# Optimization experiments

Hardware: AMD Instinct MI355X
Metric: run time of the kernel (lower is better)

The kernel has to match this reference:

```python
import jax, jax.numpy as jnp
import numpy as np

EPS = 1e-10


def setup_inputs() -> dict:
    key = jax.random.key(0)
    kS, kQ, kW, kL = jax.random.split(key, 4)
    B, C, K, Q, D = 64, 20, 5, 15, 2048
    support = jax.random.normal(kS, (B * C * K, D), dtype=jnp.float32)
    query = jax.random.normal(kQ, (B * C * Q, D), dtype=jnp.float32)
    # encoder = single Linear(in_dim=D, hidden=D)
    W = jax.random.normal(kW, (D, D), dtype=jnp.float32) / np.sqrt(D)
    b = jnp.zeros((D,), dtype=jnp.float32)
    # one-hot support labels: each class appears K times per episode
    labels = jax.random.randint(kL, (B, C * K), 0, C)
    support_label_one_hot = jax.nn.one_hot(labels, C, dtype=jnp.float32)
    return {
        "support": support,
        "query": query,
        "support_label_one_hot": support_label_one_hot,
        "W": W,
        "b": b,
        "C": C,
        "K": K,
        "Q": Q,
    }


def reference(support, query, support_label_one_hot, W, b, C, K, Q):
    H = W.shape[1]
    # encoder (linear) on flat batches
    s = (support @ W + b).reshape(-1, C * K, H)   # [B, C*K, H]
    q = (query @ W + b).reshape(-1, C * Q, H)     # [B, C*Q, H]
    # DistanceNetwork: cosine-like similarity, only support magnitude normalized
    inv_norm = jax.lax.rsqrt(jnp.clip(jnp.sum(s * s, axis=-1), EPS, None))  # [B, C*K]
    sim = jnp.einsum("bqh,bsh->bqs", q, s) * inv_norm[:, None, :]           # [B, C*Q, C*K]
    # AttentionClassify: softmax over support set, then weighted sum of one-hot labels
    att = jax.nn.softmax(sim, axis=-1)                                       # [B, C*Q, C*K]
    preds = jnp.einsum("bqs,bsc->bqc", att, support_label_one_hot)          # [B, C*Q, C]
    probs = preds.reshape(-1, C)                                             # [B*C*Q, C]
    pred = jnp.argmax(probs, axis=1)
    return probs, pred
```

## Files before the change

### kernel.cpp

```cpp
#include <hip/hip_runtime.h>
#include <hip/hip_bf16.h>
#include <math.h>

#define BATCH 64
#define NCLS  20
#define NS    100
#define NQ    300
#define DIM   2048
#define MS    (BATCH * NS)
#define MQ    (BATCH * NQ)
#define KSPL  4
#define PROW  320
#define PCOL  112

typedef __attribute__((ext_vector_type(8))) short frag_ab;
typedef __attribute__((ext_vector_type(4))) float frag_cd;

union FAB { frag_ab f; unsigned u[4]; };

__device__ __forceinline__ unsigned rne_hi(float x) {
  unsigned u = __float_as_uint(x);
  return (u + 0x7FFFu + ((u >> 16) & 1u)) & 0xFFFF0000u;
}

__device__ __forceinline__ void split2rn(float x, float y, unsigned& p1,
                                         unsigned& p2) {
  union { __hip_bfloat162 h; unsigned u; } c1, c2;
  c1.h = __float22bfloat162_rn(make_float2(x, y));
  p1 = c1.u;
  float rx = x - __uint_as_float(c1.u << 16);
  float ry = y - __uint_as_float(c1.u & 0xFFFF0000u);
  c2.h = __float22bfloat162_rn(make_float2(rx, ry));
  p2 = c2.u;
}

#define GLL16(g, l)                                                            \
  __builtin_amdgcn_global_load_lds(                                            \
      (const __attribute__((address_space(1))) void*)(g),                      \
      (__attribute__((address_space(3))) void*)(l), 16, 0, 0)

__global__ __launch_bounds__(256) void esplit2(const float* __restrict__ X,
                                               unsigned short* __restrict__ X1,
                                               unsigned short* __restrict__ X2,
                                               int n4) {
  int i = blockIdx.x * 256 + threadIdx.x;
  if (i >= n4) return;
  float4 v = ((const float4*)X)[i];
  float x[4] = {v.x, v.y, v.z, v.w};
  ushort4 o1, o2;
  unsigned short* d1 = (unsigned short*)&o1;
  unsigned short* d2 = (unsigned short*)&o2;
#pragma unroll
  for (int q = 0; q < 4; ++q) {
    unsigned u1 = rne_hi(x[q]);
    float r1 = x[q] - __uint_as_float(u1);
    unsigned u2 = rne_hi(r1);
    d1[q] = (unsigned short)(u1 >> 16);
    d2[q] = (unsigned short)(u2 >> 16);
  }
  ((ushort4*)X1)[i] = o1;
  ((ushort4*)X2)[i] = o2;
}

template <int NH, int MINW>
__global__ __launch_bounds__(256, MINW) void gemm_bb3(
    const unsigned short* __restrict__ A1, const unsigned short* __restrict__ A2,
    const unsigned short* __restrict__ B1, const unsigned short* __restrict__ B2,
    float* __restrict__ Y, unsigned short* __restrict__ S1o,
    unsigned short* __restrict__ S2o) {
  __shared__ __align__(16) unsigned short A1s[4][128][8];
  __shared__ __align__(16) unsigned short A2s[4][128][8];
  __shared__ __align__(16) unsigned short B1s[4][128 * NH][8];
  __shared__ __align__(16) unsigned short B2s[4][128 * NH][8];

  const int tid = threadIdx.x;
  const int w = tid >> 6, lane = tid & 63;
  const int ml = lane & 15, kq = lane >> 4;
  const int wm = (w >> 1) * 64, wn = (w & 1) * 64;
  const int col0 = blockIdx.x * (128 * NH), row0 = blockIdx.y * 128;

  frag_cd acc[NH][4][4];
#pragma unroll
  for (int h = 0; h < NH; ++h)
#pragma unroll
    for (int i = 0; i < 4; ++i)
#pragma unroll
      for (int j = 0; j < 4; ++j)
#pragma unroll
        for (int r = 0; r < 4; ++r) acc[h][i][j][r] = 0.f;

  for (int k0 = 0; k0 < DIM; k0 += 32) {
#pragma unroll
    for (int mh = 0; mh < 2; ++mh) {
      const size_t off = (size_t)(row0 + mh * 64 + lane) * DIM + k0 + w * 8;
      GLL16(A1 + off, &A1s[w][mh * 64][0]);
      GLL16(A2 + off, &A2s[w][mh * 64][0]);
    }
#pragma unroll
    for (int t = 0; t < 2 * NH; ++t) {
      const size_t off = (size_t)(col0 + t * 64 + lane) * DIM + k0 + w * 8;
      GLL16(B1 + off, &B1s[w][t * 64][0]);
      GLL16(B2 + off, &B2s[w][t * 64][0]);
    }
    __syncthreads();

    FAB a1[4], a2[4];
#pragma unroll
    for (int i = 0; i < 4; ++i) {
      int m = wm + i * 16 + ml;
      *(uint4*)&a1[i].u[0] = *(const uint4*)&A1s[kq][m][0];
      *(uint4*)&a2[i].u[0] = *(const uint4*)&A2s[kq][m][0];
    }
#pragma unroll
    for (int nh = 0; nh < NH; ++nh) {
#pragma unroll
      for (int j = 0; j < 4; ++j) {
        int n = nh * 128 + wn + j * 16 + ml;
        FAB b1, b2;
        *(uint4*)&b1.u[0] = *(const uint4*)&B1s[kq][n][0];
        *(uint4*)&b2.u[0] = *(const uint4*)&B2s[kq][n][0];
#pragma unroll
        for (int i = 0; i < 4; ++i) {
          acc[nh][i][j] = __builtin_amdgcn_mfma_f32_16x16x32_bf16(
              a1[i].f, b1.f, acc[nh][i][j], 0, 0, 0);
          acc[nh][i][j] = __builtin_amdgcn_mfma_f32_16x16x32_bf16(
              a1[i].f, b2.f, acc[nh][i][j], 0, 0, 0);
          acc[nh][i][j] = __builtin_amdgcn_mfma_f32_16x16x32_bf16(
              a2[i].f, b1.f, acc[nh][i][j], 0, 0, 0);
        }
      }
    }
    __syncthreads();
  }

#pragma unroll
  for (int nh = 0; nh < NH; ++nh)
#pragma unroll
    for (int j = 0; j < 4; ++j) {
      int col = col0 + nh * 128 + wn + j * 16 + ml;
#pragma unroll
      for (int i = 0; i < 4; ++i) {
        int rowb = row0 + wm + i * 16 + kq * 4;
#pragma unroll
        for (int r = 0; r < 4; ++r) {
          float val = acc[nh][i][j][r];
          size_t idx = (size_t)(rowb + r) * DIM + col;
          if (Y) Y[idx] = val;
          unsigned u1 = rne_hi(val);
          float rr = val - __uint_as_float(u1);
          unsigned u2 = rne_hi(rr);
          S1o[idx] = (unsigned short)(u1 >> 16);
          S2o[idx] = (unsigned short)(u2 >> 16);
        }
      }
    }
}

#define MFMA3(ACC, A1, A2, BV1, BV2)                                           \
  ACC = __builtin_amdgcn_mfma_f32_16x16x32_bf16(A1.f, BV1.f, ACC, 0, 0, 0);    \
  ACC = __builtin_amdgcn_mfma_f32_16x16x32_bf16(A1.f, BV2.f, ACC, 0, 0, 0);    \
  ACC = __builtin_amdgcn_mfma_f32_16x16x32_bf16(A2.f, BV1.f, ACC, 0, 0, 0)

#define SIMJ(J)                                                                \
  {                                                                            \
    FAB bf1, bf2;                                                              \
    *(uint4*)&bf1.u[0] = *(const uint4*)(z1b + o##J + k0);                     \
    *(uint4*)&bf2.u[0] = *(const uint4*)(z2b + o##J + k0);                     \
    MFMA3(acc##J, a1, a2, bf1, bf2);                                           \
  }

#define STJ(J)                                                                 \
  {                                                                            \
    const int n = J * 16 + ml;                                                 \
    part[pbase + 0 * PCOL + n] = acc##J[0];                                    \
    part[pbase + 1 * PCOL + n] = acc##J[1];                                    \
    part[pbase + 2 * PCOL + n] = acc##J[2];                                    \
    part[pbase + 3 * PCOL + n] = acc##J[3];                                    \
  }

__global__ __launch_bounds__(256) void sim2_part(
    const float* __restrict__ Xq, const unsigned short* __restrict__ Z1,
    const unsigned short* __restrict__ Z2, const float* __restrict__ wb,
    float* __restrict__ part, float* __restrict__ upart) {
  const int wg = blockIdx.x + 5 * blockIdx.y + 320 * blockIdx.z;
  const int swz = (wg & 7) * 160 + (wg >> 3);
  const int b = swz / 20;
  const int r20 = swz % 20;
  const int ks = r20 / 5;
  const int mt = r20 % 5;

  const int w = threadIdx.x >> 6, lane = threadIdx.x & 63;
  const int ml = lane & 15, kq = lane >> 4;

  int r = mt * 64 + w * 16 + ml;
  const int rc = r < NQ ? r : NQ - 1;
  const float* aptr = Xq + ((size_t)b * NQ + rc) * DIM + kq * 8;

  const unsigned short* z1b = Z1 + (size_t)b * NS * DIM + kq * 8;
  const unsigned short* z2b = Z2 + (size_t)b * NS * DIM + kq * 8;
  const int o0 = (0 * 16 + ml) * DIM;
  const int o1 = (1 * 16 + ml) * DIM;
  const int o2 = (2 * 16 + ml) * DIM;
  const int o3 = (3 * 16 + ml) * DIM;
  const int o4 = (4 * 16 + ml) * DIM;
  const int o5 = (5 * 16 + ml) * DIM;
  const int n6 = 6 * 16 + ml;
  const int o6 = (n6 < NS ? n6 : NS - 1) * DIM;

  frag_cd acc0 = {0.f, 0.f, 0.f, 0.f}, acc1 = {0.f, 0.f, 0.f, 0.f};
  frag_cd acc2 = {0.f, 0.f, 0.f, 0.f}, acc3 = {0.f, 0.f, 0.f, 0.f};
  frag_cd acc4 = {0.f, 0.f, 0.f, 0.f}, acc5 = {0.f, 0.f, 0.f, 0.f};
  frag_cd acc6 = {0.f, 0.f, 0.f, 0.f};
  float up = 0.f;

  const int kbeg = ks * (DIM / KSPL), kend = kbeg + DIM / KSPL;
#pragma unroll 2
  for (int k0 = kbeg; k0 < kend; k0 += 32) {
    float4 f0 = *(const float4*)(aptr + k0);
    float4 f1 = *(const float4*)(aptr + k0 + 4);
    float4 wa = *(const float4*)(wb + k0 + kq * 8);
    float4 wc = *(const float4*)(wb + k0 + kq * 8 + 4);
    up += f0.x * wa.x + f0.y * wa.y + f0.z * wa.z + f0.w * wa.w +
          f1.x * wc.x + f1.y * wc.y + f1.z * wc.z + f1.w * wc.w;
    FAB a1, a2;
    split2rn(f0.x, f0.y, a1.u[0], a2.u[0]);
    split2rn(f0.z, f0.w, a1.u[1], a2.u[1]);
    split2rn(f1.x, f1.y, a1.u[2], a2.u[2]);
    split2rn(f1.z, f1.w, a1.u[3], a2.u[3]);
    SIMJ(0); SIMJ(1); SIMJ(2); SIMJ(3); SIMJ(4); SIMJ(5); SIMJ(6);
  }

  up += __shfl_xor(up, 16, 64);
  up += __shfl_xor(up, 32, 64);
  if (lane < 16)
    upart[((size_t)ks * BATCH + b) * PROW + mt * 64 + w * 16 + ml] = up;

  const size_t pbase =
      (((size_t)ks * BATCH + b) * PROW + (mt * 64 + w * 16 + kq * 4)) * PCOL;
  STJ(0); STJ(1); STJ(2); STJ(3); STJ(4); STJ(5); STJ(6);
}

__global__ __launch_bounds__(256) void gemv_wb(const float* __restrict__ W,
                                               const float* __restrict__ b,
                                               float* __restrict__ wb,
                                               float* __restrict__ bb) {
  const int k = blockIdx.x;
  const int d0 = threadIdx.x * 8;
  float4 w0 = *(const float4*)(W + (size_t)k * DIM + d0);
  float4 w1 = *(const float4*)(W + (size_t)k * DIM + d0 + 4);
  float4 b0 = *(const float4*)(b + d0);
  float4 b1 = *(const float4*)(b + d0 + 4);
  float s = w0.x * b0.x + w0.y * b0.y + w0.z * b0.z + w0.w * b0.w +
            w1.x * b1.x + w1.y * b1.y + w1.z * b1.z + w1.w * b1.w;
#pragma unroll
  for (int off = 32; off; off >>= 1) s += __shfl_down(s, off, 64);
  __shared__ float red[4];
  if ((threadIdx.x & 63) == 0) red[threadIdx.x >> 6] = s;
  __syncthreads();
  if (threadIdx.x == 0) wb[k] = red[0] + red[1] + red[2] + red[3];
  if (k == 0) {
    float s2 = b0.x * b0.x + b0.y * b0.y + b0.z * b0.z + b0.w * b0.w +
               b1.x * b1.x + b1.y * b1.y + b1.z * b1.z + b1.w * b1.w;
#pragma unroll
    for (int off = 32; off; off >>= 1) s2 += __shfl_down(s2, off, 64);
    __syncthreads();
    if ((threadIdx.x & 63) == 0) red[threadIdx.x >> 6] = s2;
    __syncthreads();
    if (threadIdx.x == 0) bb[0] = red[0] + red[1] + red[2] + red[3];
  }
}

__global__ __launch_bounds__(256) void norm_v(const float* __restrict__ Z,
                                              const float* __restrict__ Xs,
                                              const float* __restrict__ wb,
                                              const float* __restrict__ bb,
                                              float* __restrict__ inv_norm,
                                              float* __restrict__ vv) {
  const int row = blockIdx.x;
  const int d0 = threadIdx.x * 8;
  const float* zp = Z + (size_t)row * DIM + d0;
  const float* xp = Xs + (size_t)row * DIM + d0;
  float4 z0 = *(const float4*)zp, z1 = *(const float4*)(zp + 4);
  float4 x0 = *(const float4*)xp, x1 = *(const float4*)(xp + 4);
  float4 w0 = *(const float4*)(wb + d0), w1 = *(const float4*)(wb + d0 + 4);
  float s1 = z0.x * x0.x + z0.y * x0.y + z0.z * x0.z + z0.w * x0.w +
             z1.x * x1.x + z1.y * x1.y + z1.z * x1.z + z1.w * x1.w;
  float s2 = x0.x * w0.x + x0.y * w0.y + x0.z * w0.z + x0.w * w0.w +
             x1.x * w1.x + x1.y * w1.y + x1.z * w1.z + x1.w * w1.w;
#pragma unroll
  for (int off = 32; off; off >>= 1) {
    s1 += __shfl_down(s1, off, 64);
    s2 += __shfl_down(s2, off, 64);
  }
  __shared__ float r1[4], r2[4];
  if ((threadIdx.x & 63) == 0) {
    r1[threadIdx.x >> 6] = s1;
    r2[threadIdx.x >> 6] = s2;
  }
  __syncthreads();
  if (threadIdx.x == 0) {
    float t1 = r1[0] + r1[1] + r1[2] + r1[3];
    float t2 = r2[0] + r2[1] + r2[2] + r2[3];
    float nn = t1 + 2.f * t2 + bb[0];
    inv_norm[row] = rsqrtf(fmaxf(nn, 1e-10f));
    vv[row] = t2;
  }
}

__global__ __launch_bounds__(256) void softmax_part(
    const float* __restrict__ part, const float* __restrict__ upart,
    const float* __restrict__ vv, const float* __restrict__ bb,
    const float* __restrict__ inv_norm, const float* __restrict__ onehot,
    float* __restrict__ out) {
  const int wave = threadIdx.x >> 6;
  const int lane = threadIdx.x & 63;
  const int r = blockIdx.x * 4 + wave;
  const int b = r / NQ;
  const int m = r - b * NQ;
  const size_t kstr = (size_t)BATCH * PROW * PCOL;
  const size_t ustr = (size_t)BATCH * PROW;
  const float* p0 = part + ((size_t)b * PROW + m) * PCOL;
  const float* up0 = upart + (size_t)b * PROW + m;
  const float bbv = bb[0];
  const float ur = up0[0] + up0[ustr] + up0[2 * ustr] + up0[3 * ustr];

  float raw1 = p0[lane] + p0[kstr + lane] + p0[2 * kstr + lane] +
               p0[3 * kstr + lane];
  float v1 = (raw1 + ur + vv[b * NS + lane] + bbv) * inv_norm[b * NS + lane];
  float v2 = -INFINITY;
  if (lane < NS - 64) {
    const int n = lane + 64;
    float raw2 = p0[n] + p0[kstr + n] + p0[2 * kstr + n] + p0[3 * kstr + n];
    v2 = (raw2 + ur + vv[b * NS + n] + bbv) * inv_norm[b * NS + n];
  }
  float mx = fmaxf(v1, v2);
#pragma unroll
  for (int off = 32; off; off >>= 1) mx = fmaxf(mx, __shfl_xor(mx, off, 64));
  float e1 = expf(v1 - mx);
  float e2 = (lane < NS - 64) ? expf(v2 - mx) : 0.f;
  float ssum = e1 + e2;
#pragma unroll
  for (int off = 32; off; off >>= 1) ssum += __shfl_xor(ssum, off, 64);
  float inv = 1.0f / ssum;
  __shared__ float att[4][NS];
  __shared__ float pr[4][NCLS];
  att[wave][lane] = e1 * inv;
  if (lane < NS - 64) att[wave][lane + 64] = e2 * inv;
  __syncthreads();
  if (lane < NCLS) {
    const float* oh = onehot + ((size_t)b * NS) * NCLS + lane;
    float p = 0.f;
#pragma unroll 4
    for (int j = 0; j < NS; ++j) p += att[wave][j] * oh[(size_t)j * NCLS];
    out[(size_t)r * NCLS + lane] = p;
    pr[wave][lane] = p;
  }
  __syncthreads();
  if (lane == 0) {
    int best = 0;
    float bv = pr[wave][0];
    for (int c = 1; c < NCLS; ++c) {
      float v = pr[wave][c];
      if (v > bv) { bv = v; best = c; }
    }
    out[(size_t)MQ * NCLS + r] = (float)best;
  }
}

__global__ __launch_bounds__(256) void softmax_fb(
    const float* __restrict__ sim, const float* __restrict__ onehot,
    float* __restrict__ out) {
  const int wave = threadIdx.x >> 6;
  const int lane = threadIdx.x & 63;
  const int r = blockIdx.x * 4 + wave;
  const int b = r / NQ;
  const float* srow = sim + (size_t)r * NS;
  float v1 = srow[lane];
  float v2 = (lane < NS - 64) ? srow[lane + 64] : -INFINITY;
  float m = fmaxf(v1, v2);
#pragma unroll
  for (int off = 32; off; off >>= 1) m = fmaxf(m, __shfl_xor(m, off, 64));
  float e1 = expf(v1 - m);
  float e2 = (lane < NS - 64) ? expf(v2 - m) : 0.f;
  float ssum = e1 + e2;
#pragma unroll
  for (int off = 32; off; off >>= 1) ssum += __shfl_xor(ssum, off, 64);
  float inv = 1.0f / ssum;
  __shared__ float att[4][NS];
  __shared__ float pr[4][NCLS];
  att[wave][lane] = e1 * inv;
  if (lane < NS - 64) att[wave][lane + 64] = e2 * inv;
  __syncthreads();
  if (lane < NCLS) {
    const float* oh = onehot + ((size_t)b * NS) * NCLS + lane;
    float p = 0.f;
#pragma unroll 4
    for (int j = 0; j < NS; ++j) p += att[wave][j] * oh[(size_t)j * NCLS];
    out[(size_t)r * NCLS + lane] = p;
    pr[wave][lane] = p;
  }
  __syncthreads();
  if (lane == 0) {
    int best = 0;
    float bv = pr[wave][0];
    for (int c = 1; c < NCLS; ++c) {
      float v = pr[wave][c];
      if (v > bv) { bv = v; best = c; }
    }
    out[(size_t)MQ * NCLS + r] = (float)best;
  }
}

__global__ __launch_bounds__(256) void gemm_xw(const float* __restrict__ X,
                                               const float* __restrict__ W,
                                               const float* __restrict__ bias,
                                               float* __restrict__ Y) {
  __shared__ float As[16][64];
  __shared__ float Bs[16][64];
  const int t = threadIdx.x;
  const int row0 = blockIdx.x * 64;
  const int col0 = blockIdx.y * 64;
  const int am = t >> 2, ak = (t & 3) * 4;
  const int bk = t >> 4, bn = (t & 15) * 4;
  const int tm = (t >> 4) * 4, tn = (t & 15) * 4;
  float acc[4][4] = {};
  for (int k0 = 0; k0 < DIM; k0 += 16) {
    float4 av = *(const float4*)(X + (size_t)(row0 + am) * DIM + k0 + ak);
    As[ak + 0][am] = av.x;
    As[ak + 1][am] = av.y;
    As[ak + 2][am] = av.z;
    As[ak + 3][am] = av.w;
    *(float4*)&Bs[bk][bn] =
        *(const float4*)(W + (size_t)(k0 + bk) * DIM + col0 + bn);
    __syncthreads();
#pragma unroll
    for (int k = 0; k < 16; ++k) {
      float4 a4 = *(const float4*)&As[k][tm];
      float4 b4 = *(const float4*)&Bs[k][tn];
      float av_[4] = {a4.x, a4.y, a4.z, a4.w};
      float bv_[4] = {b4.x, b4.y, b4.z, b4.w};
#pragma unroll
      for (int i = 0; i < 4; ++i)
#pragma unroll
        for (int j = 0; j < 4; ++j) acc[i][j] += av_[i] * bv_[j];
    }
    __syncthreads();
  }
  float4 bbv = *(const float4*)(bias + col0 + tn);
  float bv_[4] = {bbv.x, bbv.y, bbv.z, bbv.w};
#pragma unroll
  for (int i = 0; i < 4; ++i) {
    float4 o;
    o.x = acc[i][0] + bv_[0];
    o.y = acc[i][1] + bv_[1];
    o.z = acc[i][2] + bv_[2];
    o.w = acc[i][3] + bv_[3];
    *(float4*)(Y + (size_t)(row0 + tm + i) * DIM + col0 + tn) = o;
  }
}

__global__ __launch_bounds__(256) void norm_kernel(const float* __restrict__ s,
                                                   float* __restrict__ inv_norm) {
  const int row = blockIdx.x;
  const float* p = s + (size_t)row * DIM;
  const int d0 = threadIdx.x * 8;
  float4 a = *(const float4*)(p + d0);
  float4 b = *(const float4*)(p + d0 + 4);
  float sum = a.x * a.x + a.y * a.y + a.z * a.z + a.w * a.w +
              b.x * b.x + b.y * b.y + b.z * b.z + b.w * b.w;
#pragma unroll
  for (int off = 32; off; off >>= 1) sum += __shfl_down(sum, off, 64);
  __shared__ float red[4];
  if ((threadIdx.x & 63) == 0) red[threadIdx.x >> 6] = sum;
  __syncthreads();
  if (threadIdx.x == 0) {
    float tot = red[0] + red[1] + red[2] + red[3];
    inv_norm[row] = rsqrtf(fmaxf(tot, 1e-10f));
  }
}

__global__ __launch_bounds__(256) void sim_kernel(const float* __restrict__ q,
                                                  const float* __restrict__ s,
                                                  const float* __restrict__ inv_norm,
                                                  float* __restrict__ sim) {
  __shared__ float As[16][64];
  __shared__ float Bs[16][64];
  const int t = threadIdx.x;
  const int b = blockIdx.z;
  const int row0 = blockIdx.y * 64;
  const int col0 = blockIdx.x * 64;
  const float* qb = q + (size_t)b * NQ * DIM;
  const float* sb = s + (size_t)b * NS * DIM;
  const int am = t >> 2, ak = (t & 3) * 4;
  const int tm = (t >> 4) * 4, tn = (t & 15) * 4;
  float acc[4][4] = {};
  for (int k0 = 0; k0 < DIM; k0 += 16) {
    float4 av = make_float4(0.f, 0.f, 0.f, 0.f);
    if (row0 + am < NQ)
      av = *(const float4*)(qb + (size_t)(row0 + am) * DIM + k0 + ak);
    As[ak + 0][am] = av.x;
    As[ak + 1][am] = av.y;
    As[ak + 2][am] = av.z;
    As[ak + 3][am] = av.w;
    float4 bv = make_float4(0.f, 0.f, 0.f, 0.f);
    if (col0 + am < NS)
      bv = *(const float4*)(sb + (size_t)(col0 + am) * DIM + k0 + ak);
    Bs[ak + 0][am] = bv.x;
    Bs[ak + 1][am] = bv.y;
    Bs[ak + 2][am] = bv.z;
    Bs[ak + 3][am] = bv.w;
    __syncthreads();
#pragma unroll
    for (int k = 0; k < 16; ++k) {
      float4 a4 = *(const float4*)&As[k][tm];
      float4 b4 = *(const float4*)&Bs[k][tn];
      float av_[4] = {a4.x, a4.y, a4.z, a4.w};
      float bv_[4] = {b4.x, b4.y, b4.z, b4.w};
#pragma unroll
      for (int i = 0; i < 4; ++i)
#pragma unroll
        for (int j = 0; j < 4; ++j) acc[i][j] += av_[i] * bv_[j];
    }
    __syncthreads();
  }
#pragma unroll
  for (int i = 0; i < 4; ++i) {
    int m = row0 + tm + i;
    if (m >= NQ) continue;
#pragma unroll
    for (int j = 0; j < 4; ++j) {
      int n = col0 + tn + j;
      if (n >= NS) continue;
      sim[((size_t)b * NQ + m) * NS + n] = acc[i][j] * inv_norm[b * NS + n];
    }
  }
}

extern "C" void kernel_launch(void* const* d_in, const int* in_sizes, int n_in,
                              void* d_out, int out_size, void* d_ws,
                              size_t ws_size, hipStream_t stream) {
  const float* support = (const float*)d_in[0];
  const float* query   = (const float*)d_in[1];
  const float* onehot  = (const float*)d_in[2];
  const float* W       = (const float*)d_in[3];
  const float* bias    = (const float*)d_in[4];

  char* wsb = (char*)d_ws;

  const size_t NEED = 191228160;

  if (ws_size >= NEED) {
    float* Z              = (float*)wsb;
    unsigned short* S1    = (unsigned short*)(wsb + (size_t)52428800);
    unsigned short* S2    = (unsigned short*)(wsb + (size_t)78643200);
    unsigned short* Wr1   = (unsigned short*)(wsb + (size_t)104857600);
    unsigned short* Wr2   = (unsigned short*)(wsb + (size_t)113246208);
    unsigned short* G1    = (unsigned short*)(wsb + (size_t)121634816);
    unsigned short* G2    = (unsigned short*)(wsb + (size_t)130023424);
    unsigned short* Z1    = (unsigned short*)(wsb + (size_t)138412032);
    unsigned short* Z2    = (unsigned short*)(wsb + (size_t)164626432);
    float* part           = (float*)(wsb + (size_t)52428800);
    float* inv_norm       = (float*)(wsb + (size_t)190840832);
    float* vv             = (float*)(wsb + (size_t)190866432);
    float* wb             = (float*)(wsb + (size_t)190892032);
    float* bb             = (float*)(wsb + (size_t)190900224);
    float* upart          = (float*)(wsb + (size_t)190900480);

    esplit2<<<DIM * DIM / 1024, 256, 0, stream>>>(W, Wr1, Wr2, DIM * DIM / 4);
    esplit2<<<MS * DIM / 1024, 256, 0, stream>>>(support, S1, S2,
                                                 MS * DIM / 4);
    gemm_bb3<1, 2><<<dim3(DIM / 128, DIM / 128), 256, 0, stream>>>(
        Wr1, Wr2, Wr1, Wr2, nullptr, G1, G2);
    gemm_bb3<2, 2><<<dim3(DIM / 256, MS / 128), 256, 0, stream>>>(
        S1, S2, G1, G2, Z, Z1, Z2);
    gemv_wb<<<DIM, 256, 0, stream>>>(W, bias, wb, bb);
    norm_v<<<MS, 256, 0, stream>>>(Z, support, wb, bb, inv_norm, vv);
    sim2_part<<<dim3(5, BATCH, KSPL), 256, 0, stream>>>(query, Z1, Z2, wb,
                                                        part, upart);
    softmax_part<<<MQ / 4, 256, 0, stream>>>(part, upart, vv, bb, inv_norm,
                                             onehot, (float*)d_out);
  } else {
    float* s = (float*)wsb;
    float* q = (float*)(wsb + (size_t)52428800);
    float* inv_norm = q + (size_t)MQ * DIM;
    float* sim      = inv_norm + MS;
    gemm_xw<<<dim3(MS / 64, DIM / 64), 256, 0, stream>>>(support, W, bias, s);
    gemm_xw<<<dim3(MQ / 64, DIM / 64), 256, 0, stream>>>(query, W, bias, q);
    norm_kernel<<<MS, 256, 0, stream>>>(s, inv_norm);
    sim_kernel<<<dim3(2, 5, BATCH), 256, 0, stream>>>(q, s, inv_norm, sim);
    softmax_fb<<<MQ / 4, 256, 0, stream>>>(sim, onehot, (float*)d_out);
  }
}
```

Baseline: 747.8 us.

## Fuse W split with bias GEMV, drop fp32 Z, swizzle GEMM tiles

Merges the W bf16 split with the W·b GEMV into one kernel, so W is read once instead of twice. The support GEMM no longer writes an fp32 Z; the norm kernel instead rebuilds Z from its bf16 hi/lo pair, which removes a large write and read at a small precision cost. The GEMMs gain a grouped workgroup-index swizzle for L2 locality, and the second GEMM drops from 256-wide to 128-wide tiles while the occupancy hint rises to 4. The workspace layout shrinks accordingly.

```diff
diff --git a/kernel.cpp b/kernel.cpp
--- a/kernel.cpp
+++ b/kernel.cpp
@@ -32,6 +32,10 @@
   float ry = y - __uint_as_float(c1.u & 0xFFFF0000u);
   c2.h = __float22bfloat162_rn(make_float2(rx, ry));
   p2 = c2.u;
+}
+
+__device__ __forceinline__ float bf16_f(unsigned short s) {
+  return __uint_as_float(((unsigned)s) << 16);
 }
 
 #define GLL16(g, l)                                                            \
@@ -62,6 +66,60 @@
   ((ushort4*)X2)[i] = o2;
 }
 
+__global__ __launch_bounds__(256) void esplit2w(const float* __restrict__ W,
+                                                const float* __restrict__ b,
+                                                unsigned short* __restrict__ W1,
+                                                unsigned short* __restrict__ W2,
+                                                float* __restrict__ wb,
+                                                float* __restrict__ bb) {
+  const int row = blockIdx.x;
+  const int d0 = threadIdx.x * 8;
+  const float* wr = W + (size_t)row * DIM + d0;
+  float4 x0 = *(const float4*)wr, x1 = *(const float4*)(wr + 4);
+  float4 b0 = *(const float4*)(b + d0), b1 = *(const float4*)(b + d0 + 4);
+  float xs[8] = {x0.x, x0.y, x0.z, x0.w, x1.x, x1.y, x1.z, x1.w};
+  ushort4 o1a, o2a, o1b, o2b;
+  unsigned short* p1a = (unsigned short*)&o1a;
+  unsigned short* p2a = (unsigned short*)&o2a;
+  unsigned short* p1b = (unsigned short*)&o1b;
+  unsigned short* p2b = (unsigned short*)&o2b;
+#pragma unroll
+  for (int q = 0; q < 4; ++q) {
+    unsigned u1 = rne_hi(xs[q]);
+    float r1 = xs[q] - __uint_as_float(u1);
+    unsigned u2 = rne_hi(r1);
+    p1a[q] = (unsigned short)(u1 >> 16);
+    p2a[q] = (unsigned short)(u2 >> 16);
+    unsigned v1 = rne_hi(xs[q + 4]);
+    float r2 = xs[q + 4] - __uint_as_float(v1);
+    unsigned v2 = rne_hi(r2);
+    p1b[q] = (unsigned short)(v1 >> 16);
+    p2b[q] = (unsigned short)(v2 >> 16);
+  }
+  *(ushort4*)&W1[(size_t)row * DIM + d0] = o1a;
+  *(ushort4*)&W1[(size_t)row * DIM + d0 + 4] = o1b;
+  *(ushort4*)&W2[(size_t)row * DIM + d0] = o2a;
+  *(ushort4*)&W2[(size_t)row * DIM + d0 + 4] = o2b;
+  float s = x0.x * b0.x + x0.y * b0.y + x0.z * b0.z + x0.w * b0.w +
+            x1.x * b1.x + x1.y * b1.y + x1.z * b1.z + x1.w * b1.w;
+#pragma unroll
+  for (int off = 32; off; off >>= 1) s += __shfl_down(s, off, 64);
+  __shared__ float red[4];
+  if ((threadIdx.x & 63) == 0) red[threadIdx.x >> 6] = s;
+  __syncthreads();
+  if (threadIdx.x == 0) wb[row] = red[0] + red[1] + red[2] + red[3];
+  if (row == 0) {
+    float s2 = b0.x * b0.x + b0.y * b0.y + b0.z * b0.z + b0.w * b0.w +
+               b1.x * b1.x + b1.y * b1.y + b1.z * b1.z + b1.w * b1.w;
+#pragma unroll
+    for (int off = 32; off; off >>= 1) s2 += __shfl_down(s2, off, 64);
+    __syncthreads();
+    if ((threadIdx.x & 63) == 0) red[threadIdx.x >> 6] = s2;
+    __syncthreads();
+    if (threadIdx.x == 0) bb[0] = red[0] + red[1] + red[2] + red[3];
+  }
+}
+
 template <int NH, int MINW>
 __global__ __launch_bounds__(256, MINW) void gemm_bb3(
     const unsigned short* __restrict__ A1, const unsigned short* __restrict__ A2,
@@ -77,7 +135,14 @@
   const int w = tid >> 6, lane = tid & 63;
   const int ml = lane & 15, kq = lane >> 4;
   const int wm = (w >> 1) * 64, wn = (w & 1) * 64;
-  const int col0 = blockIdx.x * (128 * NH), row0 = blockIdx.y * 128;
+
+  const int nwgx = gridDim.x;
+  const int nwg = nwgx * gridDim.y;
+  const int wg = blockIdx.x + nwgx * blockIdx.y;
+  const int qq = nwg >> 3;
+  const int swz = (wg & 7) * qq + (wg >> 3);
+  const int col0 = (swz % nwgx) * (128 * NH);
+  const int row0 = (swz / nwgx) * 128;
 
   frag_cd acc[NH][4][4];
 #pragma unroll
@@ -240,51 +305,24 @@
   STJ(0); STJ(1); STJ(2); STJ(3); STJ(4); STJ(5); STJ(6);
 }
 
-__global__ __launch_bounds__(256) void gemv_wb(const float* __restrict__ W,
-                                               const float* __restrict__ b,
-                                               float* __restrict__ wb,
-                                               float* __restrict__ bb) {
-  const int k = blockIdx.x;
-  const int d0 = threadIdx.x * 8;
-  float4 w0 = *(const float4*)(W + (size_t)k * DIM + d0);
-  float4 w1 = *(const float4*)(W + (size_t)k * DIM + d0 + 4);
-  float4 b0 = *(const float4*)(b + d0);
-  float4 b1 = *(const float4*)(b + d0 + 4);
-  float s = w0.x * b0.x + w0.y * b0.y + w0.z * b0.z + w0.w * b0.w +
-            w1.x * b1.x + w1.y * b1.y + w1.z * b1.z + w1.w * b1.w;
-#pragma unroll
-  for (int off = 32; off; off >>= 1) s += __shfl_down(s, off, 64);
-  __shared__ float red[4];
-  if ((threadIdx.x & 63) == 0) red[threadIdx.x >> 6] = s;
-  __syncthreads();
-  if (threadIdx.x == 0) wb[k] = red[0] + red[1] + red[2] + red[3];
-  if (k == 0) {
-    float s2 = b0.x * b0.x + b0.y * b0.y + b0.z * b0.z + b0.w * b0.w +
-               b1.x * b1.x + b1.y * b1.y + b1.z * b1.z + b1.w * b1.w;
-#pragma unroll
-    for (int off = 32; off; off >>= 1) s2 += __shfl_down(s2, off, 64);
-    __syncthreads();
-    if ((threadIdx.x & 63) == 0) red[threadIdx.x >> 6] = s2;
-    __syncthreads();
-    if (threadIdx.x == 0) bb[0] = red[0] + red[1] + red[2] + red[3];
-  }
-}
-
-__global__ __launch_bounds__(256) void norm_v(const float* __restrict__ Z,
-                                              const float* __restrict__ Xs,
-                                              const float* __restrict__ wb,
-                                              const float* __restrict__ bb,
-                                              float* __restrict__ inv_norm,
-                                              float* __restrict__ vv) {
+__global__ __launch_bounds__(256) void norm_v2(
+    const unsigned short* __restrict__ Z1, const unsigned short* __restrict__ Z2,
+    const float* __restrict__ Xs, const float* __restrict__ wb,
+    const float* __restrict__ bb, float* __restrict__ inv_norm,
+    float* __restrict__ vv) {
   const int row = blockIdx.x;
   const int d0 = threadIdx.x * 8;
-  const float* zp = Z + (size_t)row * DIM + d0;
+  union { uint4 u; unsigned short s[8]; } z1v, z2v;
+  z1v.u = *(const uint4*)(Z1 + (size_t)row * DIM + d0);
+  z2v.u = *(const uint4*)(Z2 + (size_t)row * DIM + d0);
   const float* xp = Xs + (size_t)row * DIM + d0;
-  float4 z0 = *(const float4*)zp, z1 = *(const float4*)(zp + 4);
   float4 x0 = *(const float4*)xp, x1 = *(const float4*)(xp + 4);
   float4 w0 = *(const float4*)(wb + d0), w1 = *(const float4*)(wb + d0 + 4);
-  float s1 = z0.x * x0.x + z0.y * x0.y + z0.z * x0.z + z0.w * x0.w +
-             z1.x * x1.x + z1.y * x1.y + z1.z * x1.z + z1.w * x1.w;
+  float xs[8] = {x0.x, x0.y, x0.z, x0.w, x1.x, x1.y, x1.z, x1.w};
+  float s1 = 0.f;
+#pragma unroll
+  for (int i = 0; i < 8; ++i)
+    s1 += (bf16_f(z1v.s[i]) + bf16_f(z2v.s[i])) * xs[i];
   float s2 = x0.x * w0.x + x0.y * w0.y + x0.z * w0.z + x0.w * w0.w +
              x1.x * w1.x + x1.y * w1.y + x1.z * w1.z + x1.w * w1.w;
 #pragma unroll
@@ -547,34 +585,32 @@
 
   char* wsb = (char*)d_ws;
 
-  const size_t NEED = 191228160;
+  const size_t NEED = 175499520;
 
   if (ws_size >= NEED) {
-    float* Z              = (float*)wsb;
-    unsigned short* S1    = (unsigned short*)(wsb + (size_t)52428800);
-    unsigned short* S2    = (unsigned short*)(wsb + (size_t)78643200);
-    unsigned short* Wr1   = (unsigned short*)(wsb + (size_t)104857600);
-    unsigned short* Wr2   = (unsigned short*)(wsb + (size_t)113246208);
-    unsigned short* G1    = (unsigned short*)(wsb + (size_t)121634816);
-    unsigned short* G2    = (unsigned short*)(wsb + (size_t)130023424);
-    unsigned short* Z1    = (unsigned short*)(wsb + (size_t)138412032);
-    unsigned short* Z2    = (unsigned short*)(wsb + (size_t)164626432);
-    float* part           = (float*)(wsb + (size_t)52428800);
-    float* inv_norm       = (float*)(wsb + (size_t)190840832);
-    float* vv             = (float*)(wsb + (size_t)190866432);
-    float* wb             = (float*)(wsb + (size_t)190892032);
-    float* bb             = (float*)(wsb + (size_t)190900224);
-    float* upart          = (float*)(wsb + (size_t)190900480);
-
-    esplit2<<<DIM * DIM / 1024, 256, 0, stream>>>(W, Wr1, Wr2, DIM * DIM / 4);
+    unsigned short* S1    = (unsigned short*)(wsb);
+    unsigned short* S2    = (unsigned short*)(wsb + (size_t)26214400);
+    unsigned short* Wr1   = (unsigned short*)(wsb + (size_t)52428800);
+    unsigned short* Wr2   = (unsigned short*)(wsb + (size_t)60817408);
+    unsigned short* G1    = (unsigned short*)(wsb + (size_t)69206016);
+    unsigned short* G2    = (unsigned short*)(wsb + (size_t)77594624);
+    unsigned short* Z1    = (unsigned short*)(wsb + (size_t)85983232);
+    unsigned short* Z2    = (unsigned short*)(wsb + (size_t)112197632);
+    float* part           = (float*)(wsb + (size_t)138412032);
+    float* inv_norm       = (float*)(wsb + (size_t)175112192);
+    float* vv             = (float*)(wsb + (size_t)175137792);
+    float* wb             = (float*)(wsb + (size_t)175163392);
+    float* bb             = (float*)(wsb + (size_t)175171584);
+    float* upart          = (float*)(wsb + (size_t)175171840);
+
+    esplit2w<<<DIM, 256, 0, stream>>>(W, bias, Wr1, Wr2, wb, bb);
     esplit2<<<MS * DIM / 1024, 256, 0, stream>>>(support, S1, S2,
                                                  MS * DIM / 4);
-    gemm_bb3<1, 2><<<dim3(DIM / 128, DIM / 128), 256, 0, stream>>>(
+    gemm_bb3<1, 4><<<dim3(DIM / 128, DIM / 128), 256, 0, stream>>>(
         Wr1, Wr2, Wr1, Wr2, nullptr, G1, G2);
-    gemm_bb3<2, 2><<<dim3(DIM / 256, MS / 128), 256, 0, stream>>>(
-        S1, S2, G1, G2, Z, Z1, Z2);
-    gemv_wb<<<DIM, 256, 0, stream>>>(W, bias, wb, bb);
-    norm_v<<<MS, 256, 0, stream>>>(Z, support, wb, bb, inv_norm, vv);
+    gemm_bb3<1, 4><<<dim3(DIM / 128, MS / 128), 256, 0, stream>>>(
+        S1, S2, G1, G2, nullptr, Z1, Z2);
+    norm_v2<<<MS, 256, 0, stream>>>(Z1, Z2, support, wb, bb, inv_norm, vv);
     sim2_part<<<dim3(5, BATCH, KSPL), 256, 0, stream>>>(query, Z1, Z2, wb,
                                                         part, upart);
     softmax_part<<<MQ / 4, 256, 0, stream>>>(part, upart, vv, bb, inv_norm,
```

After: 970.7 us. +29.8%, slower.
